# Performance work log

Hardware: AMD Instinct MI355X
Metric: run time of the kernel (lower is better)

## Reference

```python
import jax, jax.numpy as jnp
import numpy as np
import math

B, T, V, D, H = 64, 128, 25, 256, 8
HD = D // H  # head_dim = 32
LN_EPS = 1e-5
NORM_EPS = 1e-12  # F.normalize default eps


def _layernorm(x, g, b):
    m = jnp.mean(x, axis=-1, keepdims=True)
    v = jnp.mean(jnp.square(x - m), axis=-1, keepdims=True)
    return (x - m) * jax.lax.rsqrt(v + LN_EPS) * g + b


def setup_inputs() -> dict:
    key = jax.random.key(0)
    ks = jax.random.split(key, 10)
    s = 0.02
    return {
        "x": jax.random.normal(ks[0], (B, T, V, D), dtype=jnp.float32),
        "ln1_g": jnp.ones((D,), jnp.float32),
        "ln1_b": jnp.zeros((D,), jnp.float32),
        "qkv_w": jax.random.normal(ks[1], (D, 3 * D), jnp.float32) * s,
        "qkv_b": jnp.zeros((3 * D,), jnp.float32),
        "proj_w": jax.random.normal(ks[2], (D, D), jnp.float32) * s,
        "proj_b": jnp.zeros((D,), jnp.float32),
        "logit_scale": jnp.full((H, 1, 1), math.log(math.sqrt(HD)), jnp.float32),
        "ln2_g": jnp.ones((D,), jnp.float32),
        "ln2_b": jnp.zeros((D,), jnp.float32),
        "ffn_w1": jax.random.normal(ks[3], (D, 4 * D), jnp.float32) * s,
        "ffn_b1": jnp.zeros((4 * D,), jnp.float32),
        "ffn_w2": jax.random.normal(ks[4], (4 * D, D), jnp.float32) * s,
        "ffn_b2": jnp.zeros((D,), jnp.float32),
    }


def reference(x, ln1_g, ln1_b, qkv_w, qkv_b, proj_w, proj_b, logit_scale,
              ln2_g, ln2_b, ffn_w1, ffn_b1, ffn_w2, ffn_b2):
    b, t, v, dm = x.shape
    n = b * t
    h, d = H, HD
    xf = x.reshape(n, v, dm)
    residual = xf
    y = _layernorm(xf, ln1_g, ln1_b)
    qkv = (y @ qkv_w + qkv_b).reshape(n, v, 3, h, d)
    qkv = jnp.transpose(qkv, (2, 0, 3, 1, 4))  # (3, n, h, v, d)
    q, k, val = qkv[0], qkv[1], qkv[2]
    # cosine attention: L2-normalize q/k, learned per-head temperature (clamped at 100)
    scale = jnp.exp(jnp.minimum(logit_scale, math.log(100.0)))  # (h,1,1)
    q = q / jnp.maximum(jnp.linalg.norm(q, axis=-1, keepdims=True), NORM_EPS) * scale[None]
    k = k / jnp.maximum(jnp.linalg.norm(k, axis=-1, keepdims=True), NORM_EPS)
    # SDPA applies its default 1/sqrt(head_dim) scaling on top
    logits = jnp.einsum('nhqd,nhkd->nhqk', q, k) / math.sqrt(d)
    attn = jax.nn.softmax(logits, axis=-1)
    out = jnp.einsum('nhqk,nhkd->nhqd', attn, val)
    out = jnp.transpose(out, (0, 2, 1, 3)).reshape(n, v, dm)
    out = out @ proj_w + proj_b
    xf = residual + out
    y2 = _layernorm(xf, ln2_g, ln2_b)
    ffn = jax.nn.gelu(y2 @ ffn_w1 + ffn_b1, approximate=False) @ ffn_w2 + ffn_b2
    xf = xf + ffn
    return xf.reshape(b, t, v, dm)
```

## Files before the change

### kernel.cpp

```cpp
#include <hip/hip_runtime.h>
#include <stdint.h>

typedef unsigned short u16;
typedef __attribute__((ext_vector_type(8))) short short8;
typedef __attribute__((ext_vector_type(4))) float f32x4;

__device__ __forceinline__ float bf2f(u16 v) {
  union { uint32_t u; float f; } x; x.u = ((uint32_t)v) << 16; return x.f;
}
__device__ __forceinline__ u16 f2bf(float f) {
  union { float f; uint32_t u; } x; x.f = f;
  uint32_t u = x.u;
  return (u16)((u + 0x7fffu + ((u >> 16) & 1u)) >> 16);
}
__device__ __forceinline__ void unp8(int4 r, float* f) {
  f[0] = __uint_as_float(((uint32_t)r.x) << 16);
  f[1] = __uint_as_float(((uint32_t)r.x) & 0xffff0000u);
  f[2] = __uint_as_float(((uint32_t)r.y) << 16);
  f[3] = __uint_as_float(((uint32_t)r.y) & 0xffff0000u);
  f[4] = __uint_as_float(((uint32_t)r.z) << 16);
  f[5] = __uint_as_float(((uint32_t)r.z) & 0xffff0000u);
  f[6] = __uint_as_float(((uint32_t)r.w) << 16);
  f[7] = __uint_as_float(((uint32_t)r.w) & 0xffff0000u);
}

#if defined(__has_builtin) && __has_builtin(__builtin_amdgcn_exp2f)
#define EXP2F(x) __builtin_amdgcn_exp2f(x)
#else
#define EXP2F(x) exp2f(x)
#endif
#if defined(__has_builtin) && __has_builtin(__builtin_amdgcn_rcpf)
#define RCPF(x) __builtin_amdgcn_rcpf(x)
#else
#define RCPF(x) (1.0f / (x))
#endif
__device__ __forceinline__ float gelu_f(float u) {
  float e = EXP2F(u * fmaf(0.044715f * u, u, 1.0f) * 2.3022082f);
  return u - u * RCPF(e + 1.0f);
}

__device__ __forceinline__ void copy16(const u16* g, u16* l) {
#if defined(__has_builtin) && __has_builtin(__builtin_amdgcn_global_load_lds)
  uintptr_t li = (uintptr_t)l;
  uintptr_t gi = (uintptr_t)g;
  __builtin_amdgcn_global_load_lds((const __attribute__((address_space(1))) uint32_t*)gi,
                                   (__attribute__((address_space(3))) uint32_t*)li, 16, 0, 0);
#else
  *(int4*)l = *(const int4*)g;
#endif
}

__global__ __launch_bounds__(256) void k0_prep(const float* __restrict__ qkvw,
                                               const float* __restrict__ projw,
                                               const float* __restrict__ w1,
                                               const float* __restrict__ w2,
                                               u16* __restrict__ wbuf) {
  int idx = blockIdx.x * 256 + threadIdx.x;
  if (idx < 196608) {
    int nn = idx >> 8, kk = idx & 255;
    wbuf[idx] = f2bf(qkvw[kk * 768 + nn]);
  } else if (idx < 262144) {
    int i = idx - 196608; int nn = i >> 8, kk = i & 255;
    wbuf[idx] = f2bf(projw[kk * 256 + nn]);
  } else if (idx < 524288) {
    int i = idx - 262144; int nn = i >> 8, kk = i & 255;
    wbuf[idx] = f2bf(w1[kk * 1024 + nn]);
  } else {
    int i = idx - 524288; int nn = i >> 10, kk = i & 1023;
    wbuf[idx] = f2bf(w2[kk * 256 + nn]);
  }
}

__global__ __launch_bounds__(256) void k1_ln1(const float* __restrict__ x,
                                              const float* __restrict__ g,
                                              const float* __restrict__ b,
                                              u16* __restrict__ Y, int row0) {
  int t = threadIdx.x; int lr = t >> 6; int lane = t & 63;
  size_t row = (size_t)blockIdx.x * 4 + lr;
  const float4 xv = *(const float4*)&x[((size_t)row0 + row) * 256 + lane * 4];
  float s = xv.x + xv.y + xv.z + xv.w;
  float q = xv.x * xv.x + xv.y * xv.y + xv.z * xv.z + xv.w * xv.w;
  #pragma unroll
  for (int off = 32; off > 0; off >>= 1) { s += __shfl_xor(s, off); q += __shfl_xor(q, off); }
  float mean = s * (1.0f / 256.0f);
  float var  = q * (1.0f / 256.0f) - mean * mean;
  float rstd = rsqrtf(var + 1e-5f);
  const float4 gv = *(const float4*)&g[lane * 4];
  const float4 bv = *(const float4*)&b[lane * 4];
  float y0 = (xv.x - mean) * rstd * gv.x + bv.x;
  float y1 = (xv.y - mean) * rstd * gv.y + bv.y;
  float y2 = (xv.z - mean) * rstd * gv.z + bv.z;
  float y3 = (xv.w - mean) * rstd * gv.w + bv.w;
  uint2 r;
  r.x = (uint32_t)f2bf(y0) | ((uint32_t)f2bf(y1) << 16);
  r.y = (uint32_t)f2bf(y2) | ((uint32_t)f2bf(y3) << 16);
  *(uint2*)&Y[row * 256 + lane * 4] = r;
}

template <int NB, bool GELU>
__global__ __launch_bounds__(256) void kA_gemm(const u16* __restrict__ A, const u16* __restrict__ Bw,
                                               const float* __restrict__ bias, u16* __restrict__ C) {
  __shared__ u16 Al[64 * 256];
  __shared__ u16 Bl[2][128 * 32];
  const int t = threadIdx.x, w = t >> 6, lane = t & 63, quad = lane >> 4, lrow = lane & 15, l7 = lane & 7;
  const int wm = w >> 1, wn = w & 1;
  const int mb = blockIdx.x * 64;
  #pragma unroll
  for (int r = 0; r < 8; r++) {
    int c = r * 256 + t;
    int row = c >> 5, q = (c & 31) ^ (row & 7);
    copy16(A + (size_t)(mb + row) * 256 + q * 8, Al + (size_t)(r * 256 + w * 64) * 8);
  }
  #pragma unroll
  for (int r = 0; r < 2; r++) {
    int c = r * 256 + t;
    copy16(Bw + (size_t)(c >> 2) * 256 + (c & 3) * 8, Bl[0] + (size_t)(r * 256 + w * 64) * 8);
  }
  __syncthreads();
  constexpr int JMAX = NB * 8;
  constexpr int LDC = NB * 128;
  f32x4 acc[2][4];
  for (int j = 0; j < JMAX; j++) {
    const int nb = j >> 3, kc = j & 7;
    if (kc == 0) {
      #pragma unroll
      for (int i = 0; i < 2; i++)
        #pragma unroll
        for (int jj = 0; jj < 4; jj++) acc[i][jj] = f32x4{0.f, 0.f, 0.f, 0.f};
    }
    if (j + 1 < JMAX) {
      const int nb1 = (j + 1) >> 3, kc1 = (j + 1) & 7;
      u16* nxtB = Bl[(j + 1) & 1];
      #pragma unroll
      for (int r = 0; r < 2; r++) {
        int c = r * 256 + t;
        copy16(Bw + (size_t)(nb1 * 128 + (c >> 2)) * 256 + kc1 * 32 + (c & 3) * 8,
               nxtB + (size_t)(r * 256 + w * 64) * 8);
      }
    }
    const u16* curB = Bl[j & 1];
    short8 af[2], bfr[4];
    #pragma unroll
    for (int mt = 0; mt < 2; mt++) {
      int row = wm * 32 + mt * 16 + lrow;
      af[mt] = *(const short8*)&Al[row * 256 + (((kc * 4 + quad) ^ l7) * 8)];
    }
    #pragma unroll
    for (int nt = 0; nt < 4; nt++)
      bfr[nt] = *(const short8*)&curB[(wn * 64 + nt * 16 + lrow) * 32 + quad * 8];
    #pragma unroll
    for (int mt = 0; mt < 2; mt++)
      #pragma unroll
      for (int nt = 0; nt < 4; nt++)
        acc[mt][nt] = __builtin_amdgcn_mfma_f32_16x16x32_bf16(af[mt], bfr[nt], acc[mt][nt], 0, 0, 0);
    __syncthreads();
    if (kc == 7) {
      #pragma unroll
      for (int nt = 0; nt < 4; nt++) {
        int n = nb * 128 + wn * 64 + nt * 16 + lrow;
        float bv = bias[n];
        #pragma unroll
        for (int mt = 0; mt < 2; mt++)
          #pragma unroll
          for (int i = 0; i < 4; i++) {
            int m = mb + wm * 32 + mt * 16 + quad * 4 + i;
            float u = acc[mt][nt][i] + bv;
            if (GELU) u = gelu_f(u);
            C[(size_t)m * LDC + n] = f2bf(u);
          }
      }
    }
  }
}

__global__ __launch_bounds__(256) void k3_attn(const u16* __restrict__ QKV,
                                               const float* __restrict__ lscale,
                                               u16* __restrict__ O) {
  __shared__ u16 Kl[8192];
  __shared__ u16 Vt[10304];
  __shared__ u16 Pl[4][1280];
  __shared__ float invk[256];

  const int n = blockIdx.x;
  const int t = threadIdx.x;
  const int w = t >> 6, lane = t & 63, quad = lane >> 4, l15 = lane & 15;
  const size_t n25 = (size_t)n * 25;

  #pragma unroll
  for (int r = 0; r < 4; r++) {
    int c = r * 256 + t;
    if (c < 800) {
      int vr = c >> 5, ci = c & 31;
      const u16* gp = QKV + (n25 + vr) * 768 + 256 + (size_t)((ci ^ (vr & 7)) * 8);
      u16* lp = Kl + (size_t)(r * 256 + w * 64) * 8;
      copy16(gp, lp);
    }
  }
  #pragma unroll
  for (int r = 0; r < 4; r++) {
    int c = r * 256 + t;
    if (c < 800) {
      int vr = c >> 5, ci = c & 31, h = ci >> 2, d8 = (ci & 3) * 8;
      int4 rv = *(const int4*)&QKV[(n25 + vr) * 768 + 512 + ci * 8];
      int base = h * 1288 + d8 * 40 + vr;
      Vt[base +   0] = (u16)((uint32_t)rv.x & 0xffffu);
      Vt[base +  40] = (u16)((uint32_t)rv.x >> 16);
      Vt[base +  80] = (u16)((uint32_t)rv.y & 0xffffu);
      Vt[base + 120] = (u16)((uint32_t)rv.y >> 16);
      Vt[base + 160] = (u16)((uint32_t)rv.z & 0xffffu);
      Vt[base + 200] = (u16)((uint32_t)rv.z >> 16);
      Vt[base + 240] = (u16)((uint32_t)rv.w & 0xffffu);
      Vt[base + 280] = (u16)((uint32_t)rv.w >> 16);
    }
  }
  {
    int h = t >> 5, d = t & 31;
    int base = h * 1288 + d * 40 + 25;
    #pragma unroll
    for (int j = 0; j < 7; j++) Vt[base + j] = 0;
  }
  __syncthreads();

  if (t < 200) {
    int h = (t * 41) >> 10;
    int vr = t - h * 25;
    float ss = 0.f;
    #pragma unroll
    for (int q = 0; q < 4; q++) {
      int chunk = (h * 4 + q) ^ (vr & 7);
      int4 rv = *(const int4*)&Kl[vr * 256 + chunk * 8];
      float f[8]; unp8(rv, f);
      #pragma unroll
      for (int j = 0; j < 8; j++) ss += f[j] * f[j];
    }
    invk[h * 32 + vr] = 1.0f / fmaxf(sqrtf(ss), 1e-12f);
  } else {
    int u = t - 200;
    int h = (u * 37) >> 8;
    int j = u - h * 7;
    invk[h * 32 + 25 + j] = 0.f;
  }
  __syncthreads();

  const u16* qbase = QKV + n25 * 768;
  const f32x4 zz = {0.f, 0.f, 0.f, 0.f};
  #pragma unroll
  for (int hh = 0; hh < 2; hh++) {
    const int h = w * 2 + hh;
    const float sc = expf(fminf(lscale[h], 4.6051701859880913680f));

    short8 af0 = *(const short8*)(qbase + (size_t)l15 * 768 + h * 32 + quad * 8);
    short8 af1 = *(const short8*)(qbase + (size_t)(16 + l15) * 768 + h * 32 + quad * 8);
    short8 bf0 = *(const short8*)&Kl[l15 * 256 + (((h * 4 + quad) ^ (l15 & 7)) * 8)];
    short8 bf1 = *(const short8*)&Kl[(16 + l15) * 256 + (((h * 4 + quad) ^ ((16 + l15) & 7)) * 8)];
    f32x4 sA[2][2];
    sA[0][0] = __builtin_amdgcn_mfma_f32_16x16x32_bf16(af0, bf0, zz, 0, 0, 0);
    sA[0][1] = __builtin_amdgcn_mfma_f32_16x16x32_bf16(af0, bf1, zz, 0, 0, 0);
    sA[1][0] = __builtin_amdgcn_mfma_f32_16x16x32_bf16(af1, bf0, zz, 0, 0, 0);
    sA[1][1] = __builtin_amdgcn_mfma_f32_16x16x32_bf16(af1, bf1, zz, 0, 0, 0);

    float ss0 = 0.f, ss1 = 0.f;
    #pragma unroll
    for (int j = 0; j < 8; j++) {
      float f0 = bf2f((u16)af0[j]); ss0 += f0 * f0;
      float f1 = bf2f((u16)af1[j]); ss1 += f1 * f1;
    }
    ss0 += __shfl_xor(ss0, 16); ss0 += __shfl_xor(ss0, 32);
    ss1 += __shfl_xor(ss1, 16); ss1 += __shfl_xor(ss1, 32);
    float fct0 = sc / (fmaxf(sqrtf(ss0), 1e-12f) * 5.6568542494923802f);
    float fct1 = sc / (fmaxf(sqrtf(ss1), 1e-12f) * 5.6568542494923802f);

    const float ik0 = invk[h * 32 + l15];
    const float ik1 = invk[h * 32 + 16 + l15];
    const bool v1 = l15 < 9;

    #pragma unroll
    for (int qt = 0; qt < 2; qt++) {
      #pragma unroll
      for (int i = 0; i < 4; i++) {
        float fr = __shfl(qt == 0 ? fct0 : fct1, quad * 4 + i);
        float l0 = sA[qt][0][i] * fr * ik0;
        float l1 = sA[qt][1][i] * fr * ik1;
        float m = fmaxf(l0, v1 ? l1 : -1e30f);
        #pragma unroll
        for (int o = 1; o < 16; o <<= 1) m = fmaxf(m, __shfl_xor(m, o));
        float e0 = expf(l0 - m);
        float e1 = v1 ? expf(l1 - m) : 0.f;
        float se = e0 + e1;
        #pragma unroll
        for (int o = 1; o < 16; o <<= 1) se += __shfl_xor(se, o);
        float inv = 1.0f / se;
        int q = qt * 16 + quad * 4 + i;
        Pl[w][q * 40 + l15]      = f2bf(e0 * inv);
        Pl[w][q * 40 + 16 + l15] = f2bf(e1 * inv);
      }
    }

    short8 pa0 = *(const short8*)&Pl[w][l15 * 40 + quad * 8];
    short8 pa1 = *(const short8*)&Pl[w][(16 + l15) * 40 + quad * 8];
    short8 vb0 = *(const short8*)&Vt[h * 1288 + l15 * 40 + quad * 8];
    short8 vb1 = *(const short8*)&Vt[h * 1288 + (16 + l15) * 40 + quad * 8];
    f32x4 oA[2][2];
    oA[0][0] = __builtin_amdgcn_mfma_f32_16x16x32_bf16(pa0, vb0, zz, 0, 0, 0);
    oA[0][1] = __builtin_amdgcn_mfma_f32_16x16x32_bf16(pa0, vb1, zz, 0, 0, 0);
    oA[1][0] = __builtin_amdgcn_mfma_f32_16x16x32_bf16(pa1, vb0, zz, 0, 0, 0);
    oA[1][1] = __builtin_amdgcn_mfma_f32_16x16x32_bf16(pa1, vb1, zz, 0, 0, 0);

    u16* ob = O + n25 * 256 + h * 32;
    #pragma unroll
    for (int qt = 0; qt < 2; qt++)
      #pragma unroll
      for (int i = 0; i < 4; i++) {
        int qr = quad * 4 + i;
        if (qt == 1 && qr >= 9) continue;
        int q = qt * 16 + qr;
        ob[(size_t)q * 256 + l15]      = f2bf(oA[qt][0][i]);
        ob[(size_t)q * 256 + 16 + l15] = f2bf(oA[qt][1][i]);
      }
  }
}

__global__ __launch_bounds__(256) void k4_proj(const u16* __restrict__ A, const u16* __restrict__ Bw,
                                               const float* __restrict__ bias,
                                               const float* __restrict__ x,
                                               const float* __restrict__ g2, const float* __restrict__ b2,
                                               u16* __restrict__ xfb, u16* __restrict__ y2b, int row0) {
  __shared__ u16 Al[64 * 256];
  __shared__ u16 Bl[2][256 * 32];
  __shared__ float ps[4][64], pq[4][64], meanv[64], rstdv[64];
  const int t = threadIdx.x, w = t >> 6, lane = t & 63, quad = lane >> 4, lrow = lane & 15, l7 = lane & 7;
  const int wn = w;
  const int mb = blockIdx.x * 64;
  #pragma unroll
  for (int r = 0; r < 8; r++) {
    int c = r * 256 + t;
    int row = c >> 5, q = (c & 31) ^ (row & 7);
    copy16(A + (size_t)(mb + row) * 256 + q * 8, Al + (size_t)(r * 256 + w * 64) * 8);
  }
  #pragma unroll
  for (int r = 0; r < 4; r++) {
    int c = r * 256 + t;
    copy16(Bw + (size_t)(c >> 2) * 256 + (c & 3) * 8, Bl[0] + (size_t)(r * 256 + w * 64) * 8);
  }
  __syncthreads();
  f32x4 acc[4][4];
  #pragma unroll
  for (int i = 0; i < 4; i++)
    #pragma unroll
    for (int j = 0; j < 4; j++) acc[i][j] = f32x4{0.f, 0.f, 0.f, 0.f};
  for (int j = 0; j < 8; j++) {
    if (j + 1 < 8) {
      u16* nxtB = Bl[(j + 1) & 1];
      #pragma unroll
      for (int r = 0; r < 4; r++) {
        int c = r * 256 + t;
        copy16(Bw + (size_t)(c >> 2) * 256 + (j + 1) * 32 + (c & 3) * 8,
               nxtB + (size_t)(r * 256 + w * 64) * 8);
      }
    }
    const u16* curB = Bl[j & 1];
    short8 af[4], bfr[4];
    #pragma unroll
    for (int mt = 0; mt < 4; mt++) {
      int row = mt * 16 + lrow;
      af[mt] = *(const short8*)&Al[row * 256 + (((j * 4 + quad) ^ l7) * 8)];
    }
    #pragma unroll
    for (int nt = 0; nt < 4; nt++)
      bfr[nt] = *(const short8*)&curB[(wn * 64 + nt * 16 + lrow) * 32 + quad * 8];
    #pragma unroll
    for (int mt = 0; mt < 4; mt++)
      #pragma unroll
      for (int nt = 0; nt < 4; nt++)
        acc[mt][nt] = __builtin_amdgcn_mfma_f32_16x16x32_bf16(af[mt], bfr[nt], acc[mt][nt], 0, 0, 0);
    __syncthreads();
  }
  #pragma unroll
  for (int nt = 0; nt < 4; nt++) {
    int nn = wn * 64 + nt * 16 + lrow;
    float bv = bias[nn];
    #pragma unroll
    for (int mt = 0; mt < 4; mt++)
      #pragma unroll
      for (int i = 0; i < 4; i++) {
        int m = mb + mt * 16 + quad * 4 + i;
        acc[mt][nt][i] += bv + x[((size_t)row0 + m) * 256 + nn];
      }
  }
  #pragma unroll
  for (int mt = 0; mt < 4; mt++)
    #pragma unroll
    for (int i = 0; i < 4; i++) {
      float s = 0.f, q = 0.f;
      #pragma unroll
      for (int nt = 0; nt < 4; nt++) { float v = acc[mt][nt][i]; s += v; q += v * v; }
      #pragma unroll
      for (int off = 1; off < 16; off <<= 1) { s += __shfl_xor(s, off); q += __shfl_xor(q, off); }
      if (lrow == 0) { int r = mt * 16 + quad * 4 + i; ps[w][r] = s; pq[w][r] = q; }
    }
  __syncthreads();
  if (t < 64) {
    float s = ps[0][t] + ps[1][t] + ps[2][t] + ps[3][t];
    float q = pq[0][t] + pq[1][t] + pq[2][t] + pq[3][t];
    float mean = s * (1.0f / 256.0f);
    float var  = q * (1.0f / 256.0f) - mean * mean;
    meanv[t] = mean; rstdv[t] = rsqrtf(var + 1e-5f);
  }
  __syncthreads();
  #pragma unroll
  for (int nt = 0; nt < 4; nt++) {
    int nn = wn * 64 + nt * 16 + lrow;
    float gg = g2[nn], bb = b2[nn];
    #pragma unroll
    for (int mt = 0; mt < 4; mt++)
      #pragma unroll
      for (int i = 0; i < 4; i++) {
        int r = mt * 16 + quad * 4 + i;
        int m = mb + r;
        float xfv = acc[mt][nt][i];
        xfb[(size_t)m * 256 + nn] = f2bf(xfv);
        y2b[(size_t)m * 256 + nn] = f2bf((xfv - meanv[r]) * rstdv[r] * gg + bb);
      }
  }
}

__global__ __launch_bounds__(256) void k6_ffn2(const u16* __restrict__ G, const u16* __restrict__ W2w,
                                               const float* __restrict__ bias,
                                               const u16* __restrict__ xfb,
                                               float* __restrict__ out, int row0) {
  __shared__ u16 Al[64 * 256];
  __shared__ u16 Bl[2][256 * 32];
  const int t = threadIdx.x, w = t >> 6, lane = t & 63, quad = lane >> 4, lrow = lane & 15, l7 = lane & 7;
  const int wn = w;
  const int mb = blockIdx.x * 64;
  #pragma unroll
  for (int r = 0; r < 4; r++) {
    int c = r * 256 + t;
    copy16(W2w + (size_t)(c >> 2) * 1024 + (c & 3) * 8, Bl[0] + (size_t)(r * 256 + w * 64) * 8);
  }
  f32x4 acc[4][4];
  #pragma unroll
  for (int i = 0; i < 4; i++)
    #pragma unroll
    for (int j = 0; j < 4; j++) acc[i][j] = f32x4{0.f, 0.f, 0.f, 0.f};
  for (int j = 0; j < 32; j++) {
    const int kch = j >> 3, kc = j & 7;
    if (kc == 0) {
      #pragma unroll
      for (int r = 0; r < 8; r++) {
        int c = r * 256 + t;
        int row = c >> 5, q = (c & 31) ^ (row & 7);
        copy16(G + (size_t)(mb + row) * 1024 + kch * 256 + q * 8,
               Al + (size_t)(r * 256 + w * 64) * 8);
      }
      __syncthreads();
    }
    if (j + 1 < 32) {
      const int kch1 = (j + 1) >> 3, kc1 = (j + 1) & 7;
      u16* nxtB = Bl[(j + 1) & 1];
      #pragma unroll
      for (int r = 0; r < 4; r++) {
        int c = r * 256 + t;
        copy16(W2w + (size_t)(c >> 2) * 1024 + kch1 * 256 + kc1 * 32 + (c & 3) * 8,
               nxtB + (size_t)(r * 256 + w * 64) * 8);
      }
    }
    const u16* curB = Bl[j & 1];
    short8 af[4], bfr[4];
    #pragma unroll
    for (int mt = 0; mt < 4; mt++) {
      int row = mt * 16 + lrow;
      af[mt] = *(const short8*)&Al[row * 256 + (((kc * 4 + quad) ^ l7) * 8)];
    }
    #pragma unroll
    for (int nt = 0; nt < 4; nt++)
      bfr[nt] = *(const short8*)&curB[(wn * 64 + nt * 16 + lrow) * 32 + quad * 8];
    #pragma unroll
    for (int mt = 0; mt < 4; mt++)
      #pragma unroll
      for (int nt = 0; nt < 4; nt++)
        acc[mt][nt] = __builtin_amdgcn_mfma_f32_16x16x32_bf16(af[mt], bfr[nt], acc[mt][nt], 0, 0, 0);
    __syncthreads();
  }
  #pragma unroll
  for (int nt = 0; nt < 4; nt++) {
    int n = wn * 64 + nt * 16 + lrow;
    float bv = bias[n];
    #pragma unroll
    for (int mt = 0; mt < 4; mt++)
      #pragma unroll
      for (int i = 0; i < 4; i++) {
        int m = mb + mt * 16 + quad * 4 + i;
        out[((size_t)row0 + m) * 256 + n] = acc[mt][nt][i] + bv + bf2f(xfb[(size_t)m * 256 + n]);
      }
  }
}

#define WEIGHT_BYTES 1572864ull

extern "C" void kernel_launch(void* const* d_in, const int* in_sizes, int n_in,
                              void* d_out, int out_size, void* d_ws, size_t ws_size,
                              hipStream_t stream) {
  const float* x     = (const float*)d_in[0];
  const float* ln1g  = (const float*)d_in[1];
  const float* ln1b  = (const float*)d_in[2];
  const float* qkvw  = (const float*)d_in[3];
  const float* qkvb  = (const float*)d_in[4];
  const float* projw = (const float*)d_in[5];
  const float* projb = (const float*)d_in[6];
  const float* lsc   = (const float*)d_in[7];
  const float* ln2g  = (const float*)d_in[8];
  const float* ln2b  = (const float*)d_in[9];
  const float* w1    = (const float*)d_in[10];
  const float* b1    = (const float*)d_in[11];
  const float* w2    = (const float*)d_in[12];
  const float* b2    = (const float*)d_in[13];
  float* out = (float*)d_out;
  char* wsb = (char*)d_ws;

  u16* wbuf = (u16*)wsb;
  u16* WQ = wbuf;
  u16* WP = wbuf + 196608;
  u16* W1 = wbuf + 262144;
  u16* W2 = wbuf + 524288;

  size_t avail = ws_size > WEIGHT_BYTES ? ws_size - WEIGHT_BYTES : 0;
  int nchunks = 64;
  for (int c = 1; c <= 64; c <<= 1) {
    size_t Rr = 204800u / (unsigned)c;
    if (Rr * 5632ull <= avail) { nchunks = c; break; }
  }
  const int R = 204800 / nchunks;
  char* cb = wsb + WEIGHT_BYTES;
  u16* Ybuf = (u16*)(cb);
  u16* QKVb = (u16*)(cb + (size_t)R * 512);
  u16* Obuf = (u16*)(cb + (size_t)R * 2048);
  u16* XFb  = (u16*)(cb + (size_t)R * 2560);
  u16* Y2b  = (u16*)(cb + (size_t)R * 3072);
  u16* Gbuf = (u16*)(cb + (size_t)R * 3584);

  k0_prep<<<3072, 256, 0, stream>>>(qkvw, projw, w1, w2, wbuf);
  for (int c = 0; c < nchunks; c++) {
    int row0 = c * R;
    k1_ln1<<<R / 4, 256, 0, stream>>>(x, ln1g, ln1b, Ybuf, row0);
    kA_gemm<6, false><<<R / 64, 256, 0, stream>>>(Ybuf, WQ, qkvb, QKVb);
    k3_attn<<<R / 25, 256, 0, stream>>>(QKVb, lsc, Obuf);
    k4_proj<<<R / 64, 256, 0, stream>>>(Obuf, WP, projb, x, ln2g, ln2b, XFb, Y2b, row0);
    kA_gemm<8, true><<<R / 64, 256, 0, stream>>>(Y2b, W1, b1, Gbuf);
    k6_ffn2<<<R / 64, 256, 0, stream>>>(Gbuf, W2, b2, XFb, out, row0);
  }
}
```

Measured before the change: 1.568 ms.

## Retile FFN2 GEMM to 128-row blocks with double-buffered A and B k-slices

The FFN down-projection kernel now processes 128 rows per block with a 2x2 wave layout, each wave computing 64x128. Both the activation tile and the weight tile are staged in 32-wide k-slices and double-buffered, replacing the previous full 256-wide A chunk load that stalled on a barrier. This halves weight re-reads per output row and raises MFMA work per shared-memory load, at the cost of more accumulator registers (128 floats per lane), which launch_bounds(256,2) then has to fit. R must also be divisible by 128.

```diff
diff --git a/kernel.cpp b/kernel.cpp
--- a/kernel.cpp
+++ b/kernel.cpp
@@ -424,73 +424,62 @@
   }
 }
 
-__global__ __launch_bounds__(256) void k6_ffn2(const u16* __restrict__ G, const u16* __restrict__ W2w,
-                                               const float* __restrict__ bias,
-                                               const u16* __restrict__ xfb,
-                                               float* __restrict__ out, int row0) {
-  __shared__ u16 Al[64 * 256];
-  __shared__ u16 Bl[2][256 * 32];
-  const int t = threadIdx.x, w = t >> 6, lane = t & 63, quad = lane >> 4, lrow = lane & 15, l7 = lane & 7;
-  const int wn = w;
-  const int mb = blockIdx.x * 64;
-  #pragma unroll
-  for (int r = 0; r < 4; r++) {
-    int c = r * 256 + t;
-    copy16(W2w + (size_t)(c >> 2) * 1024 + (c & 3) * 8, Bl[0] + (size_t)(r * 256 + w * 64) * 8);
-  }
-  f32x4 acc[4][4];
+__global__ __launch_bounds__(256, 2) void k6_ffn2(const u16* __restrict__ G, const u16* __restrict__ W2w,
+                                                  const float* __restrict__ bias,
+                                                  const u16* __restrict__ xfb,
+                                                  float* __restrict__ out, int row0) {
+  __shared__ u16 Asl[2][128 * 32];
+  __shared__ u16 Bsl[2][256 * 32];
+  const int t = threadIdx.x, w = t >> 6, lane = t & 63, quad = lane >> 4, lrow = lane & 15;
+  const int wm = w >> 1, wn = w & 1;
+  const int mb = blockIdx.x * 128;
+  auto stage = [&](int s, int buf) {
+    #pragma unroll
+    for (int r = 0; r < 2; r++) {
+      int c = r * 256 + t;
+      copy16(G + (size_t)(mb + (c >> 2)) * 1024 + s * 32 + (c & 3) * 8,
+             Asl[buf] + (size_t)(r * 256 + w * 64) * 8);
+    }
+    #pragma unroll
+    for (int r = 0; r < 4; r++) {
+      int c = r * 256 + t;
+      copy16(W2w + (size_t)(c >> 2) * 1024 + s * 32 + (c & 3) * 8,
+             Bsl[buf] + (size_t)(r * 256 + w * 64) * 8);
+    }
+  };
+  stage(0, 0);
+  __syncthreads();
+  f32x4 acc[4][8];
   #pragma unroll
   for (int i = 0; i < 4; i++)
     #pragma unroll
-    for (int j = 0; j < 4; j++) acc[i][j] = f32x4{0.f, 0.f, 0.f, 0.f};
-  for (int j = 0; j < 32; j++) {
-    const int kch = j >> 3, kc = j & 7;
-    if (kc == 0) {
-      #pragma unroll
-      for (int r = 0; r < 8; r++) {
-        int c = r * 256 + t;
-        int row = c >> 5, q = (c & 31) ^ (row & 7);
-        copy16(G + (size_t)(mb + row) * 1024 + kch * 256 + q * 8,
-               Al + (size_t)(r * 256 + w * 64) * 8);
-      }
-      __syncthreads();
-    }
-    if (j + 1 < 32) {
-      const int kch1 = (j + 1) >> 3, kc1 = (j + 1) & 7;
-      u16* nxtB = Bl[(j + 1) & 1];
-      #pragma unroll
-      for (int r = 0; r < 4; r++) {
-        int c = r * 256 + t;
-        copy16(W2w + (size_t)(c >> 2) * 1024 + kch1 * 256 + kc1 * 32 + (c & 3) * 8,
-               nxtB + (size_t)(r * 256 + w * 64) * 8);
-      }
-    }
-    const u16* curB = Bl[j & 1];
-    short8 af[4], bfr[4];
-    #pragma unroll
-    for (int mt = 0; mt < 4; mt++) {
-      int row = mt * 16 + lrow;
-      af[mt] = *(const short8*)&Al[row * 256 + (((kc * 4 + quad) ^ l7) * 8)];
-    }
-    #pragma unroll
-    for (int nt = 0; nt < 4; nt++)
-      bfr[nt] = *(const short8*)&curB[(wn * 64 + nt * 16 + lrow) * 32 + quad * 8];
+    for (int j = 0; j < 8; j++) acc[i][j] = f32x4{0.f, 0.f, 0.f, 0.f};
+  for (int s = 0; s < 32; s++) {
+    const int buf = s & 1;
+    if (s + 1 < 32) stage(s + 1, buf ^ 1);
+    short8 af[4], bfr[8];
     #pragma unroll
     for (int mt = 0; mt < 4; mt++)
-      #pragma unroll
-      for (int nt = 0; nt < 4; nt++)
+      af[mt] = *(const short8*)&Asl[buf][(wm * 64 + mt * 16 + lrow) * 32 + quad * 8];
+    #pragma unroll
+    for (int nt = 0; nt < 8; nt++)
+      bfr[nt] = *(const short8*)&Bsl[buf][(wn * 128 + nt * 16 + lrow) * 32 + quad * 8];
+    #pragma unroll
+    for (int mt = 0; mt < 4; mt++)
+      #pragma unroll
+      for (int nt = 0; nt < 8; nt++)
         acc[mt][nt] = __builtin_amdgcn_mfma_f32_16x16x32_bf16(af[mt], bfr[nt], acc[mt][nt], 0, 0, 0);
     __syncthreads();
   }
   #pragma unroll
-  for (int nt = 0; nt < 4; nt++) {
-    int n = wn * 64 + nt * 16 + lrow;
+  for (int nt = 0; nt < 8; nt++) {
+    int n = wn * 128 + nt * 16 + lrow;
     float bv = bias[n];
     #pragma unroll
     for (int mt = 0; mt < 4; mt++)
       #pragma unroll
       for (int i = 0; i < 4; i++) {
-        int m = mb + mt * 16 + quad * 4 + i;
+        int m = mb + wm * 64 + mt * 16 + quad * 4 + i;
         out[((size_t)row0 + m) * 256 + n] = acc[mt][nt][i] + bv + bf2f(xfb[(size_t)m * 256 + n]);
       }
   }
@@ -547,6 +536,6 @@
     k3_attn<<<R / 25, 256, 0, stream>>>(QKVb, lsc, Obuf);
     k4_proj<<<R / 64, 256, 0, stream>>>(Obuf, WP, projb, x, ln2g, ln2b, XFb, Y2b, row0);
     kA_gemm<8, true><<<R / 64, 256, 0, stream>>>(Y2b, W1, b1, Gbuf);
-    k6_ffn2<<<R / 64, 256, 0, stream>>>(Gbuf, W2, b2, XFb, out, row0);
-  }
-}
+    k6_ffn2<<<R / 128, 256, 0, stream>>>(Gbuf, W2, b2, XFb, out, row0);
+  }
+}
```

New measurement: 1.470 ms. -6.3%, faster.
